# Performance work log

Hardware: AMD Instinct MI355X
Metric: run time of the kernel (lower is better)

The kernel has to match this reference:

```python
import jax, jax.numpy as jnp
import numpy as np

B, S, D = 2, 2048, 1024
H = 16
HD = D // H  # 64


def _xavier(key, shape):
    fan_in, fan_out = shape[1], shape[0]
    a = jnp.sqrt(6.0 / (fan_in + fan_out))
    return jax.random.uniform(key, shape, jnp.float32, -a, a)


def setup_inputs() -> dict:
    key = jax.random.key(0)
    ks = jax.random.split(key, 7)
    xq = jax.random.normal(ks[0], (B, S, D), jnp.float32)
    xv = jax.random.normal(ks[1], (B, S, D), jnp.float32)
    xk = jax.random.normal(ks[2], (B, S, D), jnp.float32)
    Wq = _xavier(ks[3], (D, D)); bq = jnp.zeros((D,), jnp.float32)
    Wk = _xavier(ks[4], (D, D)); bk = jnp.zeros((D,), jnp.float32)
    Wv = _xavier(ks[5], (D, D)); bv = jnp.zeros((D,), jnp.float32)
    Wo = _xavier(ks[6], (D, D)); bo = jnp.zeros((D,), jnp.float32)
    return {"xq": xq, "xv": xv, "xk": xk,
            "Wq": Wq, "bq": bq, "Wk": Wk, "bk": bk,
            "Wv": Wv, "bv": bv, "Wo": Wo, "bo": bo}


def reference(xq, xv, xk, Wq, bq, Wk, bk, Wv, bv, Wo, bo):
    # Q/K/V projections (torch Linear: x @ W.T + b), split heads -> [B,H,S,HD]
    q = (xq @ Wq.T + bq).reshape(B, S, H, HD).transpose(0, 2, 1, 3)
    k = (xk @ Wk.T + bk).reshape(B, S, H, HD).transpose(0, 2, 1, 3)
    v = (xv @ Wv.T + bv).reshape(B, S, H, HD).transpose(0, 2, 1, 3)
    # scaled dot-product attention, no mask
    logits = jnp.einsum('bhqd,bhkd->bhqk', q, k) / jnp.sqrt(jnp.float32(HD))
    attn = jax.nn.softmax(logits, axis=-1)
    values = jnp.einsum('bhqk,bhkd->bhqd', attn, v)
    values = values.transpose(0, 2, 1, 3).reshape(B, S, D)
    return values @ Wo.T + bo
```

## Files before the change

### kernel.cpp

```cpp
#include <hip/hip_runtime.h>

typedef __bf16 bf16x8 __attribute__((ext_vector_type(8)));
typedef float f32x4 __attribute__((ext_vector_type(4)));
typedef __attribute__((address_space(1))) const unsigned char ga_t;
typedef __attribute__((address_space(3))) unsigned char la_t;

static __device__ __forceinline__ unsigned short f2b(float f) {
  union { float f; unsigned int i; } c; c.f = f;
  unsigned int r = c.i + 0x7FFFu + ((c.i >> 16) & 1u);
  return (unsigned short)(r >> 16);
}
static __device__ __forceinline__ unsigned int pack2(float a, float b) {
  unsigned int r;
  asm("v_cvt_pk_bf16_f32 %0, %1, %2" : "=v"(r) : "v"(a), "v"(b));
  return r;
}
static __device__ __forceinline__ int4 ld8f_cvt(const float* __restrict__ p) {
  float4 a = *(const float4*)p;
  float4 b = *(const float4*)(p + 4);
  uint4 u;
  u.x = pack2(a.x, a.y); u.y = pack2(a.z, a.w);
  u.z = pack2(b.x, b.y); u.w = pack2(b.z, b.w);
  return *(int4*)&u;
}
static __device__ __forceinline__ void glds16(const unsigned short* g, unsigned short* l) {
  __builtin_amdgcn_global_load_lds((ga_t*)g, (la_t*)l, 16, 0, 0);
}

__global__ __launch_bounds__(256)
void cvt_z(const float* __restrict__ s0, const float* __restrict__ s1,
           const float* __restrict__ s2, const float* __restrict__ s3,
           unsigned short* d0, unsigned short* d1,
           unsigned short* d2, unsigned short* d3, int n8) {
  const int z = blockIdx.y;
  const float* s = z == 0 ? s0 : z == 1 ? s1 : z == 2 ? s2 : s3;
  unsigned short* d = z == 0 ? d0 : z == 1 ? d1 : z == 2 ? d2 : d3;
  int idx = blockIdx.x * 256 + threadIdx.x;
  if (idx < n8) *(int4*)(d + (size_t)idx * 8) = ld8f_cvt(s + (size_t)idx * 8);
}

static __device__ __forceinline__ void gemm_core(
    const unsigned short* __restrict__ A, const unsigned short* __restrict__ W,
    unsigned short* sA, unsigned short* sB, f32x4 acc[4][4],
    int K, int m0, int n0) {
  const int tid = threadIdx.x;
  const int wave = tid >> 6, lane = tid & 63, quad = lane >> 4, l16 = lane & 15;
  const int wrow = (wave >> 1) * 64, wcol = (wave & 1) * 64;
  const int r = tid >> 2, c8 = (tid & 3) * 8;

  const unsigned short* gA0 = A + (size_t)(m0 + r) * K + c8;
  const unsigned short* gA1 = gA0 + (size_t)64 * K;
  const unsigned short* gB0 = W + (size_t)(n0 + r) * K + c8;
  const unsigned short* gB1 = gB0 + (size_t)64 * K;
  unsigned short* lA0 = sA + tid * 8;
  unsigned short* lA1 = lA0 + 2048;
  unsigned short* lB0 = sB + tid * 8;
  unsigned short* lB1 = lB0 + 2048;

  for (int k0 = 0; k0 < K; k0 += 32) {
    __syncthreads();
    glds16(gA0 + k0, lA0);
    glds16(gA1 + k0, lA1);
    glds16(gB0 + k0, lB0);
    glds16(gB1 + k0, lB1);
    __syncthreads();

    bf16x8 af[4], bfv[4];
#pragma unroll
    for (int i = 0; i < 4; ++i)
      af[i] = *(const bf16x8*)(&sA[(wrow + i * 16 + l16) * 32 + quad * 8]);
#pragma unroll
    for (int j = 0; j < 4; ++j)
      bfv[j] = *(const bf16x8*)(&sB[(wcol + j * 16 + l16) * 32 + quad * 8]);
#pragma unroll
    for (int i = 0; i < 4; ++i)
#pragma unroll
      for (int j = 0; j < 4; ++j)
        acc[i][j] = __builtin_amdgcn_mfma_f32_16x16x32_bf16(af[i], bfv[j], acc[i][j], 0, 0, 0);
  }
}

__global__ __launch_bounds__(256, 3)
void gemm_qkv(const unsigned short* __restrict__ A0p, const unsigned short* __restrict__ A1p,
              const unsigned short* __restrict__ A2p,
              const unsigned short* __restrict__ W0p, const unsigned short* __restrict__ W1p,
              const unsigned short* __restrict__ W2p,
              const float* __restrict__ b0p, const float* __restrict__ b1p,
              const float* __restrict__ b2p,
              unsigned short* __restrict__ C0p, unsigned short* __restrict__ C1p,
              unsigned short* __restrict__ C2p,
              int M, int N, int K, int zbase, float q0scale) {
  __shared__ __align__(16) unsigned short smem[8192];
  const int z = blockIdx.z + zbase;
  const unsigned short* A = z == 0 ? A0p : z == 1 ? A1p : A2p;
  const unsigned short* W = z == 0 ? W0p : z == 1 ? W1p : W2p;
  const float* bias = z == 0 ? b0p : z == 1 ? b1p : b2p;

  const int tid = threadIdx.x;
  const int wave = tid >> 6, lane = tid & 63, quad = lane >> 4, l16 = lane & 15;
  const int m0 = blockIdx.x * 128, n0 = blockIdx.y * 128;
  const int wrow = (wave >> 1) * 64, wcol = (wave & 1) * 64;

  f32x4 acc[4][4];
#pragma unroll
  for (int i = 0; i < 4; ++i)
#pragma unroll
    for (int j = 0; j < 4; ++j) acc[i][j] = (f32x4){0.f, 0.f, 0.f, 0.f};

  gemm_core(A, W, smem, smem + 4096, acc, K, m0, n0);

  if (z < 2) {
    unsigned short* C = z == 0 ? C0p : C1p;
    const float qs = (z == 0) ? q0scale : 1.0f;
#pragma unroll
    for (int j = 0; j < 4; ++j) {
      const int col = n0 + wcol + j * 16 + l16;
      const float bv = bias[col];
#pragma unroll
      for (int i = 0; i < 4; ++i)
#pragma unroll
        for (int r = 0; r < 4; ++r) {
          const int row = m0 + wrow + i * 16 + quad * 4 + r;
          C[(size_t)row * N + col] = f2b((acc[i][j][r] + bv) * qs);
        }
    }
  } else {
    __syncthreads();
    unsigned short* sT = smem + wave * 1152;
#pragma unroll
    for (int j = 0; j < 4; ++j) {
      const float bv = bias[n0 + wcol + j * 16 + l16];
#pragma unroll
      for (int i = 0; i < 4; ++i) {
        uint2 pk;
        pk.x = pack2(acc[i][j][0] + bv, acc[i][j][1] + bv);
        pk.y = pack2(acc[i][j][2] + bv, acc[i][j][3] + bv);
        *(uint2*)(&sT[l16 * 72 + i * 16 + quad * 4]) = pk;
      }
#pragma unroll
      for (int t = 0; t < 2; ++t) {
        const int nl = lane >> 2;
        const int colh = (lane & 3) * 8 + t * 32;
        int4 v = *(const int4*)(&sT[nl * 72 + colh]);
        *(int4*)(&C2p[(size_t)(n0 + wcol + j * 16 + nl) * M + m0 + wrow + colh]) = v;
      }
    }
  }
}

__global__ __launch_bounds__(256, 3)
void gemm_out(const unsigned short* __restrict__ A, const unsigned short* __restrict__ W,
              const float* __restrict__ bias, float* __restrict__ C,
              int M, int N, int K) {
  __shared__ __align__(16) unsigned short smem[8192];
  const int tid = threadIdx.x;
  const int wave = tid >> 6, lane = tid & 63, quad = lane >> 4, l16 = lane & 15;
  const int m0 = blockIdx.x * 128, n0 = blockIdx.y * 128;
  const int wrow = (wave >> 1) * 64, wcol = (wave & 1) * 64;

  f32x4 acc[4][4];
#pragma unroll
  for (int i = 0; i < 4; ++i)
#pragma unroll
    for (int j = 0; j < 4; ++j) acc[i][j] = (f32x4){0.f, 0.f, 0.f, 0.f};

  gemm_core(A, W, smem, smem + 4096, acc, K, m0, n0);

#pragma unroll
  for (int j = 0; j < 4; ++j) {
    const int col = n0 + wcol + j * 16 + l16;
    const float bv = bias[col];
#pragma unroll
    for (int i = 0; i < 4; ++i)
#pragma unroll
      for (int r = 0; r < 4; ++r) {
        const int row = m0 + wrow + i * 16 + quad * 4 + r;
        C[(size_t)row * N + col] = acc[i][j][r] + bv;
      }
  }
}

#define SEQ 2048
#define DMODEL 1024

__global__ __launch_bounds__(256, 2)
void attn_fused(const unsigned short* __restrict__ Q,
                const unsigned short* __restrict__ Km,
                const unsigned short* __restrict__ Vt,
                unsigned short* __restrict__ O) {
  __shared__ __align__(16) unsigned short sK[2][4096];
  __shared__ __align__(16) unsigned short sVt[2][4096];
  __shared__ __align__(16) unsigned short sPb[4][2304];

  const int tid = threadIdx.x;
  const int wave = tid >> 6, lane = tid & 63, quad = lane >> 4, l16 = lane & 15;
  const int qt = blockIdx.x;
  const int bh = blockIdx.y;
  const int b = bh >> 4, h = bh & 15;
  const size_t qrow0 = (size_t)b * SEQ + qt * 128;
  const size_t kvrow0 = (size_t)b * SEQ;
  const int hcol = h * 64;
  const int bofs = b * SEQ;
  const int qw = wave * 32;

  bf16x8 qa[2][2];
#pragma unroll
  for (int qi = 0; qi < 2; ++qi)
#pragma unroll
    for (int ks = 0; ks < 2; ++ks) {
      int4 v = *(const int4*)(&Q[(qrow0 + qw + qi * 16 + l16) * DMODEL + hcol + ks * 32 + quad * 8]);
      qa[qi][ks] = *(bf16x8*)&v;
    }

  bf16x8 ones;
#pragma unroll
  for (int i = 0; i < 8; ++i) ones[i] = (__bf16)1.0f;

  unsigned short* sP = sPb[wave];

  f32x4 acc[2][4], lacc[2];
#pragma unroll
  for (int qi = 0; qi < 2; ++qi) {
    lacc[qi] = (f32x4){0.f, 0.f, 0.f, 0.f};
#pragma unroll
    for (int hg = 0; hg < 4; ++hg) acc[qi][hg] = (f32x4){0.f, 0.f, 0.f, 0.f};
  }

  const unsigned short* gK0 = Km + (kvrow0 + wave * 16 + l16) * DMODEL + hcol + quad * 8;
  const unsigned short* gV0 = Vt + (size_t)(hcol + wave * 16 + l16) * 4096 + bofs + quad * 8;
  unsigned short* lK0 = &sK[0][wave * 1024 + lane * 8];
  unsigned short* lV0 = &sVt[0][wave * 1024 + lane * 8];

#pragma unroll
  for (int half = 0; half < 2; ++half) {
    glds16(gK0 + half * 32, lK0 + half * 512);
    glds16(gV0 + half * 32, lV0 + half * 512);
  }

  for (int kt = 0; kt < SEQ; kt += 64) {
    const int pb = (kt >> 6) & 1;
    __syncthreads();

    const int ktn = (kt + 64 < SEQ) ? kt + 64 : kt;
    unsigned short* lKn = lK0 + (pb ^ 1) * 4096;
    unsigned short* lVn = lV0 + (pb ^ 1) * 4096;
#pragma unroll
    for (int half = 0; half < 2; ++half) {
      glds16(gK0 + (size_t)ktn * DMODEL + half * 32, lKn + half * 512);
      glds16(gV0 + ktn + half * 32, lVn + half * 512);
    }

    f32x4 s[2][4];
#pragma unroll
    for (int qi = 0; qi < 2; ++qi)
#pragma unroll
      for (int kg = 0; kg < 4; ++kg) s[qi][kg] = (f32x4){0.f, 0.f, 0.f, 0.f};
#pragma unroll
    for (int kg = 0; kg < 4; ++kg) {
      bf16x8 kb0 = *(const bf16x8*)(&sK[pb][(kg * 2 + 0) * 512 + lane * 8]);
      bf16x8 kb1 = *(const bf16x8*)(&sK[pb][(kg * 2 + 1) * 512 + lane * 8]);
#pragma unroll
      for (int qi = 0; qi < 2; ++qi) {
        s[qi][kg] = __builtin_amdgcn_mfma_f32_16x16x32_bf16(kb0, qa[qi][0], s[qi][kg], 0, 0, 0);
        s[qi][kg] = __builtin_amdgcn_mfma_f32_16x16x32_bf16(kb1, qa[qi][1], s[qi][kg], 0, 0, 0);
      }
    }

#pragma unroll
    for (int qi = 0; qi < 2; ++qi)
#pragma unroll
      for (int kg = 0; kg < 4; ++kg) {
        float p0 = __builtin_amdgcn_exp2f(s[qi][kg][0]);
        float p1 = __builtin_amdgcn_exp2f(s[qi][kg][1]);
        float p2 = __builtin_amdgcn_exp2f(s[qi][kg][2]);
        float p3 = __builtin_amdgcn_exp2f(s[qi][kg][3]);
        uint2 pk; pk.x = pack2(p0, p1); pk.y = pack2(p2, p3);
        *(uint2*)(&sP[(qi * 16 + l16) * 72 + kg * 16 + quad * 4]) = pk;
      }

#pragma unroll
    for (int ks = 0; ks < 2; ++ks) {
      bf16x8 pa[2], vb[4];
#pragma unroll
      for (int qi = 0; qi < 2; ++qi)
        pa[qi] = *(const bf16x8*)(&sP[(qi * 16 + l16) * 72 + ks * 32 + quad * 8]);
#pragma unroll
      for (int hg = 0; hg < 4; ++hg)
        vb[hg] = *(const bf16x8*)(&sVt[pb][(hg * 2 + ks) * 512 + lane * 8]);
#pragma unroll
      for (int qi = 0; qi < 2; ++qi) {
#pragma unroll
        for (int hg = 0; hg < 4; ++hg)
          acc[qi][hg] = __builtin_amdgcn_mfma_f32_16x16x32_bf16(pa[qi], vb[hg], acc[qi][hg], 0, 0, 0);
        lacc[qi] = __builtin_amdgcn_mfma_f32_16x16x32_bf16(pa[qi], ones, lacc[qi], 0, 0, 0);
      }
    }
  }

#pragma unroll
  for (int qi = 0; qi < 2; ++qi)
#pragma unroll
    for (int r = 0; r < 4; ++r) {
      const float linv = 1.0f / lacc[qi][r];
      const size_t row = qrow0 + qw + qi * 16 + quad * 4 + r;
#pragma unroll
      for (int hg = 0; hg < 4; ++hg)
        O[row * DMODEL + hcol + hg * 16 + l16] = f2b(acc[qi][hg][r] * linv);
    }
}

extern "C" void kernel_launch(void* const* d_in, const int* in_sizes, int n_in,
                              void* d_out, int out_size, void* d_ws, size_t ws_size,
                              hipStream_t stream) {
  const float* xq = (const float*)d_in[0];
  const float* xv = (const float*)d_in[1];
  const float* xk = (const float*)d_in[2];
  const float* Wq = (const float*)d_in[3];
  const float* bq = (const float*)d_in[4];
  const float* Wk = (const float*)d_in[5];
  const float* bk = (const float*)d_in[6];
  const float* Wv = (const float*)d_in[7];
  const float* bv = (const float*)d_in[8];
  const float* Wo = (const float*)d_in[9];
  const float* bo = (const float*)d_in[10];
  float* out = (float*)d_out;

  const int S = 2048, D = 1024, M = 4096;
  const size_t MD = (size_t)M * D, DD = (size_t)D * D;
  const float SCL = 0.18033688011112042f;
  unsigned short* P = (unsigned short*)d_ws;
  dim3 bb(256);
  dim3 gg(M / 128, D / 128);

  const size_t need = (3 * MD + 4 * DD + 3 * MD) * 2;
  if (ws_size >= need) {
    unsigned short* Ab = P;
    unsigned short* Wb = Ab + 3 * MD;
    unsigned short* Qw = Wb + 4 * DD;
    unsigned short* Kw = Qw + MD;
    unsigned short* Vtw = Kw + MD;
    unsigned short* Ao = Ab;

    cvt_z<<<dim3((int)(MD / 8 / 256), 3), bb, 0, stream>>>(
        xq, xk, xv, xq, Ab, Ab + MD, Ab + 2 * MD, Ab, (int)(MD / 8));
    cvt_z<<<dim3((int)(DD / 8 / 256), 4), bb, 0, stream>>>(
        Wq, Wk, Wv, Wo, Wb, Wb + DD, Wb + 2 * DD, Wb + 3 * DD, (int)(DD / 8));
    gemm_qkv<<<dim3(M / 128, D / 128, 3), bb, 0, stream>>>(
        Ab, Ab + MD, Ab + 2 * MD, Wb, Wb + DD, Wb + 2 * DD,
        bq, bk, bv, Qw, Kw, Vtw, M, D, D, 0, SCL);
    attn_fused<<<dim3(S / 128, 32), bb, 0, stream>>>(Qw, Kw, Vtw, Ao);
    gemm_out<<<gg, bb, 0, stream>>>(Ao, Wb + 3 * DD, bo, out, M, D, D);
  } else {
    unsigned short* Ab = P;
    unsigned short* Wb = Ab + MD;
    unsigned short* Qw = Wb + DD;
    unsigned short* Kw = Qw + MD;
    unsigned short* Vtw = Kw + MD;
    unsigned short* Ao = Ab;
    const int an = (int)(MD / 8), wn = (int)(DD / 8);

    cvt_z<<<dim3(an / 256, 1), bb, 0, stream>>>(xq, xq, xq, xq, Ab, Ab, Ab, Ab, an);
    cvt_z<<<dim3(wn / 256, 1), bb, 0, stream>>>(Wq, Wq, Wq, Wq, Wb, Wb, Wb, Wb, wn);
    gemm_qkv<<<dim3(M / 128, D / 128, 1), bb, 0, stream>>>(
        Ab, Ab, Ab, Wb, Wb, Wb, bq, bq, bq, Qw, Qw, Qw, M, D, D, 0, SCL);

    cvt_z<<<dim3(an / 256, 1), bb, 0, stream>>>(xk, xk, xk, xk, Ab, Ab, Ab, Ab, an);
    cvt_z<<<dim3(wn / 256, 1), bb, 0, stream>>>(Wk, Wk, Wk, Wk, Wb, Wb, Wb, Wb, wn);
    gemm_qkv<<<dim3(M / 128, D / 128, 1), bb, 0, stream>>>(
        Ab, Ab, Ab, Wb, Wb, Wb, bk, bk, bk, Kw, Kw, Kw, M, D, D, 0, 1.0f);

    cvt_z<<<dim3(an / 256, 1), bb, 0, stream>>>(xv, xv, xv, xv, Ab, Ab, Ab, Ab, an);
    cvt_z<<<dim3(wn / 256, 1), bb, 0, stream>>>(Wv, Wv, Wv, Wv, Wb, Wb, Wb, Wb, wn);
    gemm_qkv<<<dim3(M / 128, D / 128, 1), bb, 0, stream>>>(
        Ab, Ab, Ab, Wb, Wb, Wb, bv, bv, bv, Vtw, Vtw, Vtw, M, D, D, 2, 1.0f);

    attn_fused<<<dim3(S / 128, 32), bb, 0, stream>>>(Qw, Kw, Vtw, Ao);

    cvt_z<<<dim3(wn / 256, 1), bb, 0, stream>>>(Wo, Wo, Wo, Wo, Wb, Wb, Wb, Wb, wn);
    gemm_out<<<gg, bb, 0, stream>>>(Ao, Wb, bo, out, M, D, D);
  }
}
```

Before: 231.3 us.

## Keep attention probabilities in registers via permlane swaps and halve query tile

The attention kernel now rearranges the exponentiated score tile into the MFMA A-operand layout with v_permlane32/16_swap in registers, replacing the round-trip through per-wave LDS scratch. Each workgroup now handles 64 query rows (16 per wave) instead of 128. That doubles the grid, raises the launch-bounds occupancy hint to 4, and frees LDS for more resident blocks. Block IDs are remapped so consecutive workgroups spread across heads and batches. The cost is that each K/V tile loaded into LDS is reused by half as many queries, so K/V traffic per query doubles.

```diff
diff --git a/kernel.cpp b/kernel.cpp
--- a/kernel.cpp
+++ b/kernel.cpp
@@ -14,6 +14,12 @@
   unsigned int r;
   asm("v_cvt_pk_bf16_f32 %0, %1, %2" : "=v"(r) : "v"(a), "v"(b));
   return r;
+}
+static __device__ __forceinline__ void pl32s(unsigned& a, unsigned& b) {
+  asm("v_permlane32_swap_b32 %0, %1" : "+v"(a), "+v"(b));
+}
+static __device__ __forceinline__ void pl16s(unsigned& a, unsigned& b) {
+  asm("v_permlane16_swap_b32 %0, %1" : "+v"(a), "+v"(b));
 }
 static __device__ __forceinline__ int4 ld8f_cvt(const float* __restrict__ p) {
   float4 a = *(const float4*)p;
@@ -183,48 +189,43 @@
 #define SEQ 2048
 #define DMODEL 1024
 
-__global__ __launch_bounds__(256, 2)
+__global__ __launch_bounds__(256, 4)
 void attn_fused(const unsigned short* __restrict__ Q,
                 const unsigned short* __restrict__ Km,
                 const unsigned short* __restrict__ Vt,
                 unsigned short* __restrict__ O) {
   __shared__ __align__(16) unsigned short sK[2][4096];
   __shared__ __align__(16) unsigned short sVt[2][4096];
-  __shared__ __align__(16) unsigned short sPb[4][2304];
 
   const int tid = threadIdx.x;
   const int wave = tid >> 6, lane = tid & 63, quad = lane >> 4, l16 = lane & 15;
-  const int qt = blockIdx.x;
-  const int bh = blockIdx.y;
+
+  const int nwg = gridDim.x * gridDim.y;
+  const int pid = blockIdx.y * gridDim.x + blockIdx.x;
+  const int lid = (pid & 7) * (nwg >> 3) + (pid >> 3);
+  const int qt = lid & 31;
+  const int bh = lid >> 5;
   const int b = bh >> 4, h = bh & 15;
-  const size_t qrow0 = (size_t)b * SEQ + qt * 128;
+  const size_t qrow0 = (size_t)b * SEQ + qt * 64 + wave * 16;
   const size_t kvrow0 = (size_t)b * SEQ;
   const int hcol = h * 64;
   const int bofs = b * SEQ;
-  const int qw = wave * 32;
-
-  bf16x8 qa[2][2];
-#pragma unroll
-  for (int qi = 0; qi < 2; ++qi)
-#pragma unroll
-    for (int ks = 0; ks < 2; ++ks) {
-      int4 v = *(const int4*)(&Q[(qrow0 + qw + qi * 16 + l16) * DMODEL + hcol + ks * 32 + quad * 8]);
-      qa[qi][ks] = *(bf16x8*)&v;
-    }
+
+  bf16x8 qa[2];
+#pragma unroll
+  for (int ks = 0; ks < 2; ++ks) {
+    int4 v = *(const int4*)(&Q[(qrow0 + l16) * DMODEL + hcol + ks * 32 + quad * 8]);
+    qa[ks] = *(bf16x8*)&v;
+  }
 
   bf16x8 ones;
 #pragma unroll
   for (int i = 0; i < 8; ++i) ones[i] = (__bf16)1.0f;
 
-  unsigned short* sP = sPb[wave];
-
-  f32x4 acc[2][4], lacc[2];
-#pragma unroll
-  for (int qi = 0; qi < 2; ++qi) {
-    lacc[qi] = (f32x4){0.f, 0.f, 0.f, 0.f};
-#pragma unroll
-    for (int hg = 0; hg < 4; ++hg) acc[qi][hg] = (f32x4){0.f, 0.f, 0.f, 0.f};
-  }
+  f32x4 acc[4], lacc;
+  lacc = (f32x4){0.f, 0.f, 0.f, 0.f};
+#pragma unroll
+  for (int hg = 0; hg < 4; ++hg) acc[hg] = (f32x4){0.f, 0.f, 0.f, 0.f};
 
   const unsigned short* gK0 = Km + (kvrow0 + wave * 16 + l16) * DMODEL + hcol + quad * 8;
   const unsigned short* gV0 = Vt + (size_t)(hcol + wave * 16 + l16) * 4096 + bofs + quad * 8;
@@ -250,63 +251,60 @@
       glds16(gV0 + ktn + half * 32, lVn + half * 512);
     }
 
-    f32x4 s[2][4];
-#pragma unroll
-    for (int qi = 0; qi < 2; ++qi)
-#pragma unroll
-      for (int kg = 0; kg < 4; ++kg) s[qi][kg] = (f32x4){0.f, 0.f, 0.f, 0.f};
+    f32x4 s[4];
+#pragma unroll
+    for (int kg = 0; kg < 4; ++kg) s[kg] = (f32x4){0.f, 0.f, 0.f, 0.f};
 #pragma unroll
     for (int kg = 0; kg < 4; ++kg) {
       bf16x8 kb0 = *(const bf16x8*)(&sK[pb][(kg * 2 + 0) * 512 + lane * 8]);
       bf16x8 kb1 = *(const bf16x8*)(&sK[pb][(kg * 2 + 1) * 512 + lane * 8]);
-#pragma unroll
-      for (int qi = 0; qi < 2; ++qi) {
-        s[qi][kg] = __builtin_amdgcn_mfma_f32_16x16x32_bf16(kb0, qa[qi][0], s[qi][kg], 0, 0, 0);
-        s[qi][kg] = __builtin_amdgcn_mfma_f32_16x16x32_bf16(kb1, qa[qi][1], s[qi][kg], 0, 0, 0);
-      }
-    }
-
-#pragma unroll
-    for (int qi = 0; qi < 2; ++qi)
-#pragma unroll
-      for (int kg = 0; kg < 4; ++kg) {
-        float p0 = __builtin_amdgcn_exp2f(s[qi][kg][0]);
-        float p1 = __builtin_amdgcn_exp2f(s[qi][kg][1]);
-        float p2 = __builtin_amdgcn_exp2f(s[qi][kg][2]);
-        float p3 = __builtin_amdgcn_exp2f(s[qi][kg][3]);
-        uint2 pk; pk.x = pack2(p0, p1); pk.y = pack2(p2, p3);
-        *(uint2*)(&sP[(qi * 16 + l16) * 72 + kg * 16 + quad * 4]) = pk;
-      }
-
+      s[kg] = __builtin_amdgcn_mfma_f32_16x16x32_bf16(kb0, qa[0], s[kg], 0, 0, 0);
+      s[kg] = __builtin_amdgcn_mfma_f32_16x16x32_bf16(kb1, qa[1], s[kg], 0, 0, 0);
+    }
+
+    unsigned w0[4], w1[4];
+#pragma unroll
+    for (int kg = 0; kg < 4; ++kg) {
+      float p0 = __builtin_amdgcn_exp2f(s[kg][0]);
+      float p1 = __builtin_amdgcn_exp2f(s[kg][1]);
+      float p2 = __builtin_amdgcn_exp2f(s[kg][2]);
+      float p3 = __builtin_amdgcn_exp2f(s[kg][3]);
+      w0[kg] = pack2(p0, p1);
+      w1[kg] = pack2(p2, p3);
+    }
+
+    bf16x8 pa[2];
 #pragma unroll
     for (int ks = 0; ks < 2; ++ks) {
-      bf16x8 pa[2], vb[4];
-#pragma unroll
-      for (int qi = 0; qi < 2; ++qi)
-        pa[qi] = *(const bf16x8*)(&sP[(qi * 16 + l16) * 72 + ks * 32 + quad * 8]);
+      unsigned a = w0[2 * ks], c = w0[2 * ks + 1];
+      unsigned bq = w1[2 * ks], d = w1[2 * ks + 1];
+      pl32s(a, c);  pl16s(a, c);
+      pl32s(bq, d); pl16s(bq, d);
+      uint4 u; u.x = a; u.y = bq; u.z = c; u.w = d;
+      pa[ks] = *(bf16x8*)&u;
+    }
+
+#pragma unroll
+    for (int ks = 0; ks < 2; ++ks) {
+      bf16x8 vb[4];
 #pragma unroll
       for (int hg = 0; hg < 4; ++hg)
         vb[hg] = *(const bf16x8*)(&sVt[pb][(hg * 2 + ks) * 512 + lane * 8]);
 #pragma unroll
-      for (int qi = 0; qi < 2; ++qi) {
-#pragma unroll
-        for (int hg = 0; hg < 4; ++hg)
-          acc[qi][hg] = __builtin_amdgcn_mfma_f32_16x16x32_bf16(pa[qi], vb[hg], acc[qi][hg], 0, 0, 0);
-        lacc[qi] = __builtin_amdgcn_mfma_f32_16x16x32_bf16(pa[qi], ones, lacc[qi], 0, 0, 0);
-      }
-    }
-  }
-
-#pragma unroll
-  for (int qi = 0; qi < 2; ++qi)
-#pragma unroll
-    for (int r = 0; r < 4; ++r) {
-      const float linv = 1.0f / lacc[qi][r];
-      const size_t row = qrow0 + qw + qi * 16 + quad * 4 + r;
-#pragma unroll
       for (int hg = 0; hg < 4; ++hg)
-        O[row * DMODEL + hcol + hg * 16 + l16] = f2b(acc[qi][hg][r] * linv);
-    }
+        acc[hg] = __builtin_amdgcn_mfma_f32_16x16x32_bf16(pa[ks], vb[hg], acc[hg], 0, 0, 0);
+      lacc = __builtin_amdgcn_mfma_f32_16x16x32_bf16(pa[ks], ones, lacc, 0, 0, 0);
+    }
+  }
+
+#pragma unroll
+  for (int r = 0; r < 4; ++r) {
+    const float linv = 1.0f / lacc[r];
+    const size_t row = qrow0 + quad * 4 + r;
+#pragma unroll
+    for (int hg = 0; hg < 4; ++hg)
+      O[row * DMODEL + hcol + hg * 16 + l16] = f2b(acc[hg][r] * linv);
+  }
 }
 
 extern "C" void kernel_launch(void* const* d_in, const int* in_sizes, int n_in,
@@ -348,7 +346,7 @@
     gemm_qkv<<<dim3(M / 128, D / 128, 3), bb, 0, stream>>>(
         Ab, Ab + MD, Ab + 2 * MD, Wb, Wb + DD, Wb + 2 * DD,
         bq, bk, bv, Qw, Kw, Vtw, M, D, D, 0, SCL);
-    attn_fused<<<dim3(S / 128, 32), bb, 0, stream>>>(Qw, Kw, Vtw, Ao);
+    attn_fused<<<dim3(S / 64, 32), bb, 0, stream>>>(Qw, Kw, Vtw, Ao);
     gemm_out<<<gg, bb, 0, stream>>>(Ao, Wb + 3 * DD, bo, out, M, D, D);
   } else {
     unsigned short* Ab = P;
@@ -374,7 +372,7 @@
     gemm_qkv<<<dim3(M / 128, D / 128, 1), bb, 0, stream>>>(
         Ab, Ab, Ab, Wb, Wb, Wb, bv, bv, bv, Vtw, Vtw, Vtw, M, D, D, 2, 1.0f);
 
-    attn_fused<<<dim3(S / 128, 32), bb, 0, stream>>>(Qw, Kw, Vtw, Ao);
+    attn_fused<<<dim3(S / 64, 32), bb, 0, stream>>>(Qw, Kw, Vtw, Ao);
 
     cvt_z<<<dim3(wn / 256, 1), bb, 0, stream>>>(Wo, Wo, Wo, Wo, Wb, Wb, Wb, Wb, wn);
     gemm_out<<<gg, bb, 0, stream>>>(Ao, Wb, bo, out, M, D, D);
```

Result: slower. 239.7 us (+3.7%).
